# Performance work log

Hardware: AMD Instinct MI355X
Metric: run time of the kernel (lower is better)

The kernel has to match this reference:

```python
import jax, jax.numpy as jnp
import numpy as np

# Geometry of the single LocallyConnected2d layer being decomposed
FACTOR = 2      # number of sublayers the out_channels are split into
KH = KW = 3     # kernel size
DH = DW = 1     # stride
OH = OW = 32    # output spatial size
B, C_IN, C_OUT = 128, 32, 64
H = W = OH + KH - 1  # 34 (valid unfold with stride 1)


def setup_inputs() -> dict:
    key = jax.random.key(0)
    kx, kw_, kb = jax.random.split(key, 3)
    x = jax.random.normal(kx, (B, C_IN, H, W), dtype=jnp.float32)
    # per-location weights: (out_ch, in_ch, oh, ow, kh*kw) -- no weight sharing
    weight = jax.random.normal(kw_, (C_OUT, C_IN, OH, OW, KH * KW), dtype=jnp.float32) * 0.05
    bias = jax.random.normal(kb, (C_OUT, OH, OW), dtype=jnp.float32)
    return {"x": x, "weight": weight, "bias": bias}


def _unfold(x):
    # x: (B, C, H, W) -> patches: (B, C, OH, OW, KH*KW)
    # equivalent to torch x.unfold(2,kh,dh).unfold(3,kw,dw).reshape(..., kh*kw)
    cols = [x[:, :, i:i + DH * OH:DH, j:j + DW * OW:DW]
            for i in range(KH) for j in range(KW)]
    return jnp.stack(cols, axis=-1)


def reference(x, weight, bias):
    patches = _unfold(x)  # (B, C, OH, OW, K2)
    new_ch = weight.shape[0] // FACTOR
    outs = []
    for g in range(FACTOR):  # decomposed sublayers, concatenated on channel dim
        w_g = weight[g * new_ch:(g + 1) * new_ch]
        b_g = bias[g * new_ch:(g + 1) * new_ch]
        # out[b,o,i,j] = sum_{c,k} patches[b,c,i,j,k] * w[o,c,i,j,k] + b[o,i,j]
        o_g = jnp.einsum('bcijk,ocijk->boij', patches, w_g) + b_g[None]
        outs.append(o_g)
    return jnp.concatenate(outs, axis=1)  # (B, C_OUT, OH, OW)
```

## Files before the change

### kernel.cpp

```cpp
#include <hip/hip_runtime.h>
#include <cstdint>
#include <cstddef>

#define B_    128
#define C_    32
#define O_    64
#define H_    34
#define NPOS  1024
#define K9    9
#define BC    (B_ * C_)
#define BO    (B_ * O_)
#define NPK   (NPOS * K9)

typedef __bf16 v8bf __attribute__((ext_vector_type(8)));
typedef float  v4f  __attribute__((ext_vector_type(4)));
typedef float  f4a  __attribute__((ext_vector_type(4)));

__device__ __forceinline__ unsigned short f2bf(float f) {
    union { float f; unsigned int u; } v; v.f = f;
    unsigned int u = v.u;
    return (unsigned short)((u + 0x7FFFu + ((u >> 16) & 1u)) >> 16);
}

__global__ __launch_bounds__(256) void repack_x(const float* __restrict__ x,
                                                unsigned short* __restrict__ x2) {
    const int bq = blockIdx.x / 17;
    const int hp = blockIdx.x % 17;
    const int b0 = bq * 2;
    const int h0 = hp * 2;
    __shared__ unsigned short tile[2][H_][66];
    const int t = threadIdx.x;

    for (int e = t; e < 2176; e += 256) {
        const int bb  = e / 1088;
        const int rem = e % 1088;
        const int c   = rem / 34;
        const int wp  = rem % 34;
        const float2 v = *(const float2*)(x +
            ((size_t)((b0 + bb) * C_ + c) * H_ + h0) * H_ + wp * 2);
        const int hh = (wp >= 17) ? 1 : 0;
        const int w  = wp * 2 - hh * 34;
        const int idx = bb * 32 + c;
        tile[hh][w][idx]     = f2bf(v.x);
        tile[hh][w + 1][idx] = f2bf(v.y);
    }
    __syncthreads();

    for (int e = t; e < 2176; e += 256) {
        const int hh  = e / 1088;
        const int rem = e % 1088;
        const int w   = rem >> 5;
        const int i2  = rem & 31;
        ushort2 pk;
        pk.x = tile[hh][w][i2 * 2];
        pk.y = tile[hh][w][i2 * 2 + 1];
        *(ushort2*)(x2 + (size_t)((h0 + hh) * H_ + w) * BC + bq * 64 + i2 * 2) = pk;
    }
}

__global__ __launch_bounds__(512, 2) void lc_fused5(const unsigned short* __restrict__ x2,
                                                    const float* __restrict__ weight,
                                                    const float* __restrict__ bias,
                                                    float* __restrict__ out) {
    __shared__ __align__(16) unsigned short Wl[144 * 512];

    const int bid = blockIdx.x;
    const int lb  = (bid & 7) * 32 + (bid >> 3);
    const int i   = lb >> 3;
    const int jq  = (lb >> 2) & 1;
    const int oq  = lb & 3;
    const int j0  = jq * 16;
    const int o0  = oq * 16;
    const int posbase = i * 32 + j0;
    const int t = threadIdx.x;

    const float* wbase = weight + ((size_t)(o0 * C_) * NPOS + posbase) * K9;
#pragma unroll
    for (int r = 0; r < 3; ++r) {
        f4a v[3][4];
#pragma unroll
        for (int m = 0; m < 3; ++m) {
            const int Q  = (r * 3 + m) * 512 + t;
            const int pl = Q / 9;
            const int q4 = Q % 9;
            const float* src = wbase + (size_t)pl * NPK + q4 * 16;
#pragma unroll
            for (int s = 0; s < 4; ++s)
                v[m][s] = *(const f4a*)(src + s * 4);
        }
#pragma unroll
        for (int m = 0; m < 3; ++m) {
            const int Q  = (r * 3 + m) * 512 + t;
            const int pl = Q / 9;
            const int q4 = Q % 9;
#pragma unroll
            for (int s = 0; s < 4; ++s) {
                const int d4  = q4 * 4 + s;
                const int col = ((pl >> 3) ^ (d4 & 7)) * 8 + (pl & 7);
#pragma unroll
                for (int u = 0; u < 4; ++u)
                    Wl[(d4 * 4 + u) * 512 + col] = f2bf(v[m][s][u]);
            }
        }
    }
    __syncthreads();

    const int wv = t >> 6;
    const int l  = t & 63;
    const int lm = l & 15;
    const int q  = l >> 4;

#pragma unroll
    for (int jh = 0; jh < 2; ++jh) {
        v4f acc[8];
#pragma unroll
        for (int a = 0; a < 8; ++a) acc[a] = (v4f){0.f, 0.f, 0.f, 0.f};

#pragma unroll
        for (int kh = 0; kh < 3; ++kh) {
            v8bf ax[10];
            const int rowbase = (i + kh) * H_ + j0 + jh * 8;
#pragma unroll
            for (int w6 = 0; w6 < 10; ++w6) {
                const unsigned short* xrow = x2 + (size_t)(rowbase + w6) * BC;
                ax[w6] = *(const v8bf*)(xrow + (wv * 16 + lm) * C_ + q * 8);
            }
#pragma unroll
            for (int kw = 0; kw < 3; ++kw) {
                const int tap = kh * 3 + kw;
#pragma unroll
                for (int jj = 0; jj < 8; ++jj) {
                    const int jk = (jh * 8 + jj) * K9 + tap;
                    const int gc = ((lm * 4 + q) ^ ((jk >> 2) & 7)) * 8;
                    const v8bf bfr = *(const v8bf*)&Wl[jk * 512 + gc];
                    acc[jj] = __builtin_amdgcn_mfma_f32_16x16x32_bf16(
                        ax[kw + jj], bfr, acc[jj], 0, 0, 0);
                }
            }
        }

        const float* bp = bias + (size_t)(o0 + lm) * NPOS + posbase + jh * 8;
        const f4a bv0 = *(const f4a*)bp;
        const f4a bv1 = *(const f4a*)(bp + 4);
#pragma unroll
        for (int r2 = 0; r2 < 4; ++r2) {
            const int b = wv * 16 + q * 4 + r2;
            float* op = out + ((size_t)b * O_ + (o0 + lm)) * NPOS + posbase + jh * 8;
            f4a lo = {acc[0][r2] + bv0[0], acc[1][r2] + bv0[1],
                      acc[2][r2] + bv0[2], acc[3][r2] + bv0[3]};
            f4a hi = {acc[4][r2] + bv1[0], acc[5][r2] + bv1[1],
                      acc[6][r2] + bv1[2], acc[7][r2] + bv1[3]};
            *(f4a*)op       = lo;
            *(f4a*)(op + 4) = hi;
        }
    }
}

__global__ __launch_bounds__(256) void lc_fallback(const float* __restrict__ x,
                                                   const float* __restrict__ weight,
                                                   const float* __restrict__ bias,
                                                   float* __restrict__ out) {
    const int pos = blockIdx.x;
    const int i = pos >> 5, j = pos & 31;
    const int t  = threadIdx.x;
    const int wv = t >> 6;
    const int l  = t & 63;
    const int lm = l & 15;
    const int q  = l >> 4;

    float bv[4];
#pragma unroll
    for (int nt = 0; nt < 4; ++nt)
        bv[nt] = bias[(size_t)(nt * 16 + lm) * NPOS + pos];

    v4f acc[2][4];
#pragma unroll
    for (int a = 0; a < 2; ++a)
#pragma unroll
        for (int n = 0; n < 4; ++n) acc[a][n] = (v4f){0.f, 0.f, 0.f, 0.f};

    for (int k = 0; k < K9; ++k) {
        const int kh = k / 3, kw = k % 3;
        v8bf af[2], bfr[4];
#pragma unroll
        for (int mt = 0; mt < 2; ++mt) {
            const int b = wv * 32 + mt * 16 + lm;
            union { v8bf v; unsigned short s[8]; } u;
#pragma unroll
            for (int cc = 0; cc < 8; ++cc)
                u.s[cc] = f2bf(x[(((size_t)b * C_ + q * 8 + cc) * H_ + (i + kh)) * H_ + (j + kw)]);
            af[mt] = u.v;
        }
#pragma unroll
        for (int nt = 0; nt < 4; ++nt) {
            union { v8bf v; unsigned short s[8]; } u;
#pragma unroll
            for (int cc = 0; cc < 8; ++cc) {
                const int p = (nt * 16 + lm) * C_ + q * 8 + cc;
                u.s[cc] = f2bf(weight[((size_t)p * NPOS + pos) * K9 + k]);
            }
            bfr[nt] = u.v;
        }
#pragma unroll
        for (int mt = 0; mt < 2; ++mt)
#pragma unroll
            for (int nt = 0; nt < 4; ++nt)
                acc[mt][nt] = __builtin_amdgcn_mfma_f32_16x16x32_bf16(
                    af[mt], bfr[nt], acc[mt][nt], 0, 0, 0);
    }
#pragma unroll
    for (int mt = 0; mt < 2; ++mt)
#pragma unroll
        for (int nt = 0; nt < 4; ++nt) {
            const int o = nt * 16 + lm;
#pragma unroll
            for (int r = 0; r < 4; ++r) {
                const int b = wv * 32 + mt * 16 + q * 4 + r;
                out[(size_t)(b * O_ + o) * NPOS + pos] = acc[mt][nt][r] + bv[nt];
            }
        }
}

extern "C" void kernel_launch(void* const* d_in, const int* in_sizes, int n_in,
                              void* d_out, int out_size, void* d_ws, size_t ws_size,
                              hipStream_t stream) {
    const float* x      = (const float*)d_in[0];
    const float* weight = (const float*)d_in[1];
    const float* bias   = (const float*)d_in[2];
    float* out          = (float*)d_out;

    const size_t X2B = (size_t)H_ * H_ * BC * sizeof(unsigned short);

    if (ws_size >= X2B) {
        unsigned short* x2 = (unsigned short*)d_ws;
        repack_x<<<64 * 17, 256, 0, stream>>>(x, x2);
        lc_fused5<<<256, 512, 0, stream>>>(x2, weight, bias, out);
    } else {
        lc_fallback<<<NPOS, 256, 0, stream>>>(x, weight, bias, out);
    }
}
```

Measured before the change: 158.8 us.

## Retile fused kernel to all 64 outputs by 4 positions per block

Each block now covers all 64 output channels for 4 consecutive positions, where before it covered 16 channels for 16 positions. Each loaded x fragment now feeds 4 output-channel MFMAs, and x2 re-reads across output-channel groups go away, as do the halo rows fetched per 8-position half. Weight loading changes from 64-byte to 16-byte chunks per thread, which may coalesce less well. Launch bounds drop to 1 block per CU, trading occupancy for more accumulators per thread.

```diff
diff --git a/kernel.cpp b/kernel.cpp
--- a/kernel.cpp
+++ b/kernel.cpp
@@ -58,49 +58,40 @@
     }
 }
 
-__global__ __launch_bounds__(512, 2) void lc_fused5(const unsigned short* __restrict__ x2,
+__global__ __launch_bounds__(512, 1) void lc_fused6(const unsigned short* __restrict__ x2,
                                                     const float* __restrict__ weight,
                                                     const float* __restrict__ bias,
                                                     float* __restrict__ out) {
-    __shared__ __align__(16) unsigned short Wl[144 * 512];
+    __shared__ __align__(16) unsigned short Wl[36 * 2048];
 
     const int bid = blockIdx.x;
     const int lb  = (bid & 7) * 32 + (bid >> 3);
     const int i   = lb >> 3;
-    const int jq  = (lb >> 2) & 1;
-    const int oq  = lb & 3;
-    const int j0  = jq * 16;
-    const int o0  = oq * 16;
+    const int jq  = lb & 7;
+    const int j0  = jq * 4;
     const int posbase = i * 32 + j0;
     const int t = threadIdx.x;
 
-    const float* wbase = weight + ((size_t)(o0 * C_) * NPOS + posbase) * K9;
+    const float* wbase = weight + (size_t)posbase * K9;
 #pragma unroll
     for (int r = 0; r < 3; ++r) {
-        f4a v[3][4];
-#pragma unroll
-        for (int m = 0; m < 3; ++m) {
-            const int Q  = (r * 3 + m) * 512 + t;
-            const int pl = Q / 9;
-            const int q4 = Q % 9;
-            const float* src = wbase + (size_t)pl * NPK + q4 * 16;
-#pragma unroll
-            for (int s = 0; s < 4; ++s)
-                v[m][s] = *(const f4a*)(src + s * 4);
-        }
-#pragma unroll
-        for (int m = 0; m < 3; ++m) {
-            const int Q  = (r * 3 + m) * 512 + t;
-            const int pl = Q / 9;
-            const int q4 = Q % 9;
-#pragma unroll
-            for (int s = 0; s < 4; ++s) {
-                const int d4  = q4 * 4 + s;
-                const int col = ((pl >> 3) ^ (d4 & 7)) * 8 + (pl & 7);
-#pragma unroll
-                for (int u = 0; u < 4; ++u)
-                    Wl[(d4 * 4 + u) * 512 + col] = f2bf(v[m][s][u]);
-            }
+        f4a v[12];
+#pragma unroll
+        for (int m = 0; m < 12; ++m) {
+            const int task = (r * 12 + m) * 512 + t;
+            const int pl = task / 9;
+            const int d4 = task % 9;
+            v[m] = *(const f4a*)(wbase + (size_t)pl * NPK + d4 * 4);
+        }
+#pragma unroll
+        for (int m = 0; m < 12; ++m) {
+            const int task = (r * 12 + m) * 512 + t;
+            const int pl = task / 9;
+            const int d4 = task % 9;
+            const int col = (((pl >> 3) ^ (d4 & 7)) << 3) + (pl & 7);
+#pragma unroll
+            for (int u = 0; u < 4; ++u)
+                Wl[(d4 * 4 + u) * 2048 + col] = f2bf(v[m][u]);
         }
     }
     __syncthreads();
@@ -110,48 +101,49 @@
     const int lm = l & 15;
     const int q  = l >> 4;
 
-#pragma unroll
-    for (int jh = 0; jh < 2; ++jh) {
-        v4f acc[8];
-#pragma unroll
-        for (int a = 0; a < 8; ++a) acc[a] = (v4f){0.f, 0.f, 0.f, 0.f};
-
-#pragma unroll
-        for (int kh = 0; kh < 3; ++kh) {
-            v8bf ax[10];
-            const int rowbase = (i + kh) * H_ + j0 + jh * 8;
-#pragma unroll
-            for (int w6 = 0; w6 < 10; ++w6) {
-                const unsigned short* xrow = x2 + (size_t)(rowbase + w6) * BC;
-                ax[w6] = *(const v8bf*)(xrow + (wv * 16 + lm) * C_ + q * 8);
-            }
-#pragma unroll
-            for (int kw = 0; kw < 3; ++kw) {
-                const int tap = kh * 3 + kw;
-#pragma unroll
-                for (int jj = 0; jj < 8; ++jj) {
-                    const int jk = (jh * 8 + jj) * K9 + tap;
-                    const int gc = ((lm * 4 + q) ^ ((jk >> 2) & 7)) * 8;
-                    const v8bf bfr = *(const v8bf*)&Wl[jk * 512 + gc];
-                    acc[jj] = __builtin_amdgcn_mfma_f32_16x16x32_bf16(
-                        ax[kw + jj], bfr, acc[jj], 0, 0, 0);
+    v4f acc[4][4];
+#pragma unroll
+    for (int a = 0; a < 4; ++a)
+#pragma unroll
+        for (int n = 0; n < 4; ++n) acc[a][n] = (v4f){0.f, 0.f, 0.f, 0.f};
+
+#pragma unroll
+    for (int kh = 0; kh < 3; ++kh) {
+        v8bf ax[6];
+        const int rowbase = (i + kh) * H_ + j0;
+#pragma unroll
+        for (int w6 = 0; w6 < 6; ++w6) {
+            const unsigned short* xrow = x2 + (size_t)(rowbase + w6) * BC;
+            ax[w6] = *(const v8bf*)(xrow + (wv * 16 + lm) * C_ + q * 8);
+        }
+#pragma unroll
+        for (int kw = 0; kw < 3; ++kw) {
+            const int tap = kh * 3 + kw;
+#pragma unroll
+            for (int jj = 0; jj < 4; ++jj) {
+                const int jk = jj * K9 + tap;
+                const int xr = (jk >> 2) & 7;
+#pragma unroll
+                for (int nt = 0; nt < 4; ++nt) {
+                    const int p8 = (nt * 16 + lm) * 4 + q;
+                    const v8bf bfr = *(const v8bf*)&Wl[jk * 2048 + ((p8 ^ xr) << 3)];
+                    acc[jj][nt] = __builtin_amdgcn_mfma_f32_16x16x32_bf16(
+                        ax[kw + jj], bfr, acc[jj][nt], 0, 0, 0);
                 }
             }
         }
-
-        const float* bp = bias + (size_t)(o0 + lm) * NPOS + posbase + jh * 8;
-        const f4a bv0 = *(const f4a*)bp;
-        const f4a bv1 = *(const f4a*)(bp + 4);
+    }
+
+#pragma unroll
+    for (int nt = 0; nt < 4; ++nt) {
+        const int o = nt * 16 + lm;
+        const f4a bv = *(const f4a*)(bias + (size_t)o * NPOS + posbase);
 #pragma unroll
         for (int r2 = 0; r2 < 4; ++r2) {
             const int b = wv * 16 + q * 4 + r2;
-            float* op = out + ((size_t)b * O_ + (o0 + lm)) * NPOS + posbase + jh * 8;
-            f4a lo = {acc[0][r2] + bv0[0], acc[1][r2] + bv0[1],
-                      acc[2][r2] + bv0[2], acc[3][r2] + bv0[3]};
-            f4a hi = {acc[4][r2] + bv1[0], acc[5][r2] + bv1[1],
-                      acc[6][r2] + bv1[2], acc[7][r2] + bv1[3]};
-            *(f4a*)op       = lo;
-            *(f4a*)(op + 4) = hi;
+            f4a val = {acc[0][nt][r2] + bv[0], acc[1][nt][r2] + bv[1],
+                       acc[2][nt][r2] + bv[2], acc[3][nt][r2] + bv[3]};
+            *(f4a*)(out + ((size_t)b * O_ + o) * NPOS + posbase) = val;
         }
     }
 }
@@ -234,7 +226,7 @@
     if (ws_size >= X2B) {
         unsigned short* x2 = (unsigned short*)d_ws;
         repack_x<<<64 * 17, 256, 0, stream>>>(x, x2);
-        lc_fused5<<<256, 512, 0, stream>>>(x2, weight, bias, out);
+        lc_fused6<<<256, 512, 0, stream>>>(x2, weight, bias, out);
     } else {
         lc_fallback<<<NPOS, 256, 0, stream>>>(x, weight, bias, out);
     }
```

Result: no change. 160.3 us (+1.0%).
